# Kernel optimization log

Hardware: AMD Instinct MI355X
Metric: run time of the kernel (lower is better)

The kernel has to match this reference:

```python
import jax, jax.numpy as jnp
import numpy as np

NUM_CLASSES = 80
TOPK = 1000
CONF_THRESH = 0.001
NMS_THRESH = 0.5
CLASS_OFFSET = 4096.0  # > max image coordinate, separates classes for class-aware NMS
M = 300000


def setup_inputs() -> dict:
    key = jax.random.key(0)
    k1, k2, k3, k4 = jax.random.split(key, 4)
    obj_preds = jax.random.normal(k1, (1, M, 1), dtype=jnp.float32)
    cls_preds = jax.random.normal(k2, (1, M, NUM_CLASSES), dtype=jnp.float32)
    # random xyxy boxes inside a 640x640 image
    cxcy = jax.random.uniform(k3, (1, M, 2), dtype=jnp.float32) * 640.0
    wh = jax.random.uniform(k4, (1, M, 2), dtype=jnp.float32) * 128.0 + 1.0
    box_preds = jnp.concatenate([cxcy - wh * 0.5, cxcy + wh * 0.5], axis=-1)
    return {"obj_preds": obj_preds, "cls_preds": cls_preds, "box_preds": box_preds}


def _iou_matrix(boxes):
    # boxes: [K, 4] xyxy -> [K, K] pairwise IoU
    x1, y1, x2, y2 = boxes[:, 0], boxes[:, 1], boxes[:, 2], boxes[:, 3]
    area = jnp.clip(x2 - x1, 0.0) * jnp.clip(y2 - y1, 0.0)
    xx1 = jnp.maximum(x1[:, None], x1[None, :])
    yy1 = jnp.maximum(y1[:, None], y1[None, :])
    xx2 = jnp.minimum(x2[:, None], x2[None, :])
    yy2 = jnp.minimum(y2[:, None], y2[None, :])
    inter = jnp.clip(xx2 - xx1, 0.0) * jnp.clip(yy2 - yy1, 0.0)
    return inter / (area[:, None] + area[None, :] - inter + 1e-9)


def _postprocess(obj_preds, cls_preds, box_preds):
    obj = obj_preds[0]   # [M, 1]
    cls = cls_preds[0]   # [M, C]
    box = box_preds[0]   # [M, 4]

    # sigmoid * sigmoid sqrt-score fusion (no_multi_labels branch)
    fused = jnp.sqrt(jax.nn.sigmoid(obj) * jax.nn.sigmoid(cls))  # [M, C]
    scores = jnp.max(fused, axis=1)     # [M]
    labels = jnp.argmax(fused, axis=1)  # [M]

    # sort-descending + take top-k == lax.top_k
    topk_scores, topk_idxs = jax.lax.top_k(scores, TOPK)
    labels_k = labels[topk_idxs]        # [K]
    boxes_k = box[topk_idxs]            # [K, 4]
    conf_mask = topk_scores > CONF_THRESH

    # multiclass NMS via class-offset trick (boxes of different classes never overlap)
    off = labels_k.astype(boxes_k.dtype)[:, None] * CLASS_OFFSET
    iou = _iou_matrix(boxes_k + off)    # [K, K]

    idx = jnp.arange(TOPK)

    def body(i, keep):
        # suppressed if any earlier, still-kept box overlaps > nms_thresh
        sup = (iou[i] > NMS_THRESH) & keep & (idx < i)
        return keep.at[i].set(keep[i] & ~jnp.any(sup))

    keep = jax.lax.fori_loop(0, TOPK, body, conf_mask)  # [K] bool

    keepf = keep.astype(topk_scores.dtype)
    # fixed-shape output: masked [K, 5] = (score, x1, y1, x2, y2); dropped rows zeroed
    out5 = jnp.concatenate([(topk_scores * keepf)[:, None], boxes_k * keepf[:, None]], axis=1)
    return out5, labels_k, keep


def reference(obj_preds, cls_preds, box_preds):
    return _postprocess(obj_preds, cls_preds, box_preds)
```

## Files before the change

### kernel.cpp

```cpp
#include <hip/hip_runtime.h>
#include <hip/hip_bf16.h>
#include <math.h>

#define NCLS 80
#define TOPK_N 1000
#define CAND_CAP 12288
#define T0 0.91f
#define OBJ_T 1.55f
#define NB 8192
#define HREP 8
#define RBINS 3072
#define RBIN_LO 0x3F680000u
#define ANCH_INV 524287

#define WS_CAND     0
#define WS_TKSCORE  98304
#define WS_TKANCH   102304
#define WS_TKLABEL  106304
#define WS_BOXES    110304
#define WS_OBX      126304
#define WS_AREAS    142304
#define WS_MASK     146304
#define WS_META     274304
#define WS_HIST     274368

typedef unsigned long long u64;

__device__ __forceinline__ float sigmoidf_(float x) {
    return 1.0f / (1.0f + expf(-x));
}

__device__ __forceinline__ u64 make_key2(unsigned s32, int anchor) {
    return ((u64)s32 << 19) | (unsigned)(ANCH_INV - anchor);
}

__device__ __forceinline__ int key_bin(u64 k) {
    unsigned s32 = (unsigned)(k >> 19);
    int d = (int)(s32 - RBIN_LO);
    if (d < 0) d = 0;
    int b = d >> 9;
    if (b > RBINS - 1) b = RBINS - 1;
    return (RBINS - 1) - b;
}

__device__ __forceinline__ void rowmax16(const float4* row, int l,
                                         float& bv, int& bc) {
    float4 v4 = row[l];
    bv = v4.x; bc = l * 4;
    if (v4.y > bv) { bv = v4.y; bc = l * 4 + 1; }
    if (v4.z > bv) { bv = v4.z; bc = l * 4 + 2; }
    if (v4.w > bv) { bv = v4.w; bc = l * 4 + 3; }
    if (l < 4) {
        float4 w4 = row[16 + l];
        int cb = 64 + l * 4;
        if (w4.x > bv) { bv = w4.x; bc = cb; }
        if (w4.y > bv) { bv = w4.y; bc = cb + 1; }
        if (w4.z > bv) { bv = w4.z; bc = cb + 2; }
        if (w4.w > bv) { bv = w4.w; bc = cb + 3; }
    }
    #pragma unroll
    for (int m = 8; m >= 1; m >>= 1) {
        float ov = __shfl_xor(bv, m);
        int oc = __shfl_xor(bc, m);
        if (ov > bv || (ov == bv && oc < bc)) { bv = ov; bc = oc; }
    }
}

__global__ void __launch_bounds__(256)
k1_scores(const float* __restrict__ obj,
          const float* __restrict__ cls,
          u64* __restrict__ cand,
          int* __restrict__ counter,
          unsigned* __restrict__ hist,
          int M) {
    __shared__ int lcount, lbase, nsurv;
    __shared__ int sanch[256];
    __shared__ float sobj[256];
    __shared__ u64 lkeys[256];
    int t = threadIdx.x;
    if (t == 0) { lcount = 0; nsurv = 0; }
    for (int i = blockIdx.x * 256 + t; i < (HREP * NB) / 4; i += gridDim.x * 256)
        ((uint4*)hist)[i] = make_uint4(0u, 0u, 0u, 0u);
    __syncthreads();
    int a = blockIdx.x * 256 + t;
    float o = (a < M) ? obj[a] : -1e30f;
    if (o > OBJ_T) {
        int p = atomicAdd(&nsurv, 1);
        sanch[p] = a; sobj[p] = o;
    }
    __syncthreads();
    int ns = nsurv;
    int grp = t >> 4, l = t & 15;
    for (int s = grp; s < ns; s += 16) {
        int anchor = sanch[s];
        const float4* p = (const float4*)(cls + (size_t)anchor * NCLS);
        float4 v = p[l];
        float m = fmaxf(fmaxf(v.x, v.y), fmaxf(v.z, v.w));
        if (l < 4) {
            float4 w4 = p[16 + l];
            m = fmaxf(m, fmaxf(fmaxf(w4.x, w4.y), fmaxf(w4.z, w4.w)));
        }
        #pragma unroll
        for (int sh = 8; sh >= 1; sh >>= 1)
            m = fmaxf(m, __shfl_xor(m, sh));
        if (l == 0) {
            float score = sqrtf(sigmoidf_(sobj[s]) * sigmoidf_(m));
            if (score > T0) {
                int pos = atomicAdd(&lcount, 1);
                lkeys[pos] = make_key2(__float_as_uint(score), anchor);
            }
        }
    }
    __syncthreads();
    if (t == 0 && lcount > 0) lbase = atomicAdd(counter, lcount);
    __syncthreads();
    int n = lcount;
    if (t < n) {
        int pos = lbase + t;
        if (pos < CAND_CAP) cand[pos] = lkeys[t];
    }
}

__global__ void __launch_bounds__(256)
kfb_fallback(const float* __restrict__ obj,
             const float* __restrict__ cls,
             unsigned* __restrict__ hist,
             int* __restrict__ meta,
             u64* __restrict__ cand, int M) {
    int C = meta[2];
    if (C >= TOPK_N && C <= CAND_CAP) return;
    int t = threadIdx.x;
    int gw = (blockIdx.x * 256 + t) >> 6;
    int TW = gridDim.x * 4;
    int lane64 = t & 63;
    int g = lane64 >> 4, l = lane64 & 15;
    int rep = blockIdx.x & (HREP - 1);
    for (int a0 = gw * 4; a0 < M; a0 += TW * 4) {
        int anchor = a0 + g;
        if (anchor >= M) continue;
        const float4* row = (const float4*)(cls + (size_t)anchor * NCLS);
        float bv; int bc;
        rowmax16(row, l, bv, bc);
        if (l == 0) {
            float score = sqrtf(sigmoidf_(obj[anchor]) * sigmoidf_(bv));
            atomicAdd(&hist[(size_t)rep * NB + (__float_as_uint(score) >> 17)], 1u);
        }
    }
    __threadfence();
    __shared__ bool last;
    if (t == 0)
        last = (atomicAdd(meta + 4, 1) == (int)gridDim.x - 1);
    __syncthreads();
    if (last) {
        int lane = t & 63, w = t >> 6;
        int base = NB - 1 - t * 32;
        unsigned bins[32]; unsigned s = 0;
        #pragma unroll
        for (int k = 0; k < 32; ++k) {
            unsigned h = 0;
            for (int r = 0; r < HREP; ++r)
                h += atomicOr(&hist[(size_t)r * NB + base - k], 0u);
            bins[k] = h; s += h;
        }
        unsigned inc = s;
        for (int d = 1; d < 64; d <<= 1) {
            unsigned pv = __shfl_up(inc, d);
            if (lane >= d) inc += pv;
        }
        __shared__ unsigned wsum[4], woff[4];
        if (lane == 63) wsum[w] = inc;
        __syncthreads();
        if (t == 0) {
            unsigned cum = 0;
            for (int i = 0; i < 4; ++i) { woff[i] = cum; cum += wsum[i]; }
        }
        __syncthreads();
        unsigned excl = woff[w] + inc - s;
        if (excl < TOPK_N && excl + s >= TOPK_N) {
            unsigned cum = excl; int b = base;
            #pragma unroll
            for (int k = 0; k < 32; ++k) {
                unsigned h = bins[k];
                if (cum + h >= TOPK_N) { atomicExch(meta + 0, b); break; }
                cum += h; --b;
            }
        }
        __syncthreads();
        __threadfence();
        if (t == 0) atomicExch(meta + 5, 1);
    }
    if (t == 0)
        while (atomicAdd(meta + 5, 0) == 0) { __builtin_amdgcn_s_sleep(8); }
    __syncthreads();
    __threadfence();
    int B = atomicAdd(meta + 0, 0);
    for (int a0 = gw * 4; a0 < M; a0 += TW * 4) {
        int anchor = a0 + g;
        if (anchor >= M) continue;
        const float4* row = (const float4*)(cls + (size_t)anchor * NCLS);
        float bv; int bc;
        rowmax16(row, l, bv, bc);
        if (l == 0) {
            float score = sqrtf(sigmoidf_(obj[anchor]) * sigmoidf_(bv));
            unsigned key = __float_as_uint(score);
            if ((int)(key >> 17) >= B) {
                int pos = atomicAdd(meta + 3, 1);
                if (pos < CAND_CAP)
                    cand[pos] = make_key2(key, anchor);
            }
        }
    }
}

__global__ void __launch_bounds__(1024)
k4_rank(const u64* __restrict__ cand,
        const int* __restrict__ meta,
        float* __restrict__ tkscore,
        int* __restrict__ tkanchor) {
    __shared__ u64 sorted[CAND_CAP];
    __shared__ unsigned hist[RBINS];
    __shared__ unsigned cnt[RBINS];
    __shared__ unsigned wsum[16], woff[16];
    int t = threadIdx.x;
    int lane = t & 63, w = t >> 6;
    int Cf = meta[2];
    bool fast = (Cf >= TOPK_N && Cf <= CAND_CAP);
    int C = fast ? Cf : meta[3];
    if (C > CAND_CAP) C = CAND_CAP;
    for (int b = t; b < RBINS; b += 1024) { hist[b] = 0; cnt[b] = 0; }
    __syncthreads();
    u64 keys[12]; int nk = 0;
    for (int i = t; i < C; i += 1024) {
        u64 k = cand[i];
        keys[nk++] = k;
        atomicAdd(&hist[key_bin(k)], 1u);
    }
    __syncthreads();
    unsigned h0 = hist[t * 3], h1 = hist[t * 3 + 1], h2 = hist[t * 3 + 2];
    unsigned s = h0 + h1 + h2;
    unsigned inc = s;
    for (int d = 1; d < 64; d <<= 1) {
        unsigned pv = __shfl_up(inc, d);
        if (lane >= d) inc += pv;
    }
    if (lane == 63) wsum[w] = inc;
    __syncthreads();
    if (t == 0) {
        unsigned cum = 0;
        for (int i = 0; i < 16; ++i) { woff[i] = cum; cum += wsum[i]; }
    }
    __syncthreads();
    unsigned base = woff[w] + inc - s;
    hist[t * 3] = base;
    hist[t * 3 + 1] = base + h0;
    hist[t * 3 + 2] = base + h0 + h1;
    __syncthreads();
    nk = 0;
    for (int i = t; i < C; i += 1024) {
        u64 k = keys[nk++];
        int b = key_bin(k);
        unsigned pos = hist[b] + atomicAdd(&cnt[b], 1u);
        sorted[pos] = k;
    }
    __syncthreads();
    for (int p = t; p < C; p += 1024) {
        u64 k = sorted[p];
        int b = key_bin(k);
        unsigned b0 = hist[b], b1 = b0 + cnt[b];
        int r = (int)b0;
        for (unsigned q = b0; q < b1; ++q) r += (sorted[q] > k);
        if (r < TOPK_N) {
            tkscore[r] = __uint_as_float((unsigned)(k >> 19));
            tkanchor[r] = ANCH_INV - (int)(k & 0x7FFFF);
        }
    }
}

__global__ void __launch_bounds__(256)
k4b_gather(const float* __restrict__ cls,
           const float4* __restrict__ box,
           const int* __restrict__ tkanchor,
           int* __restrict__ tklabel,
           float4* __restrict__ boxes_k,
           float4* __restrict__ obx,
           float* __restrict__ areas) {
    int grp = threadIdx.x >> 4, l = threadIdx.x & 15;
    int r = blockIdx.x * 16 + grp;
    if (r >= TOPK_N) return;
    int anchor = tkanchor[r];
    const float4* row = (const float4*)(cls + (size_t)anchor * NCLS);
    float bv; int bc;
    rowmax16(row, l, bv, bc);
    if (l == 0) {
        tklabel[r] = bc;
        float4 b = box[anchor];
        boxes_k[r] = b;
        float off = (float)bc * 4096.0f;
        float4 ob = make_float4(b.x + off, b.y + off, b.z + off, b.w + off);
        obx[r] = ob;
        areas[r] = fmaxf(ob.z - ob.x, 0.0f) * fmaxf(ob.w - ob.y, 0.0f);
    }
}

__global__ void __launch_bounds__(1024)
k5_iou(const float4* __restrict__ obx,
       const float* __restrict__ areas,
       u64* __restrict__ mask) {
    __shared__ float4 sobx[TOPK_N];
    __shared__ float  sarea[TOPK_N];
    int t = threadIdx.x;
    for (int j = t; j < TOPK_N; j += 1024) { sobx[j] = obx[j]; sarea[j] = areas[j]; }
    __syncthreads();
    int w = t >> 6, lane = t & 63;
    int i = blockIdx.x * 16 + w;
    if (i >= TOPK_N) return;
    float4 bi = sobx[i];
    float ai = sarea[i];
    #pragma unroll 4
    for (int q = 0; q < 16; ++q) {
        int c = q * 64 + lane;
        bool bit = false;
        if (c < i) {
            float4 bc = sobx[c];
            float xx1 = fmaxf(bi.x, bc.x), yy1 = fmaxf(bi.y, bc.y);
            float xx2 = fminf(bi.z, bc.z), yy2 = fminf(bi.w, bc.w);
            float inter = fmaxf(xx2 - xx1, 0.0f) * fmaxf(yy2 - yy1, 0.0f);
            float iou = inter / (ai + sarea[c] - inter + 1e-9f);
            bit = iou > 0.5f;
        }
        u64 bal = __ballot(bit);
        if (lane == 0) mask[(size_t)i * 16 + q] = bal;
    }
}

__global__ void __launch_bounds__(1024)
k6_nms(const float* __restrict__ tkscore,
       const u64* __restrict__ mask,
       const int* __restrict__ tklabel,
       const float4* __restrict__ boxes_k,
       float* __restrict__ out) {
    __shared__ u64 kept_s[16], dec_s[16];
    int t = threadIdx.x, w = t >> 6, lane = t & 63;
    bool active = t < TOPK_N;
    u64 sup[16];
    float sc = 0.0f;
    if (active) {
        #pragma unroll
        for (int q = 0; q < 16; ++q) sup[q] = mask[(size_t)t * 16 + q];
        sc = tkscore[t];
    } else {
        #pragma unroll
        for (int q = 0; q < 16; ++q) sup[q] = 0ULL;
    }
    bool conf = active && (sc > 0.001f);
    bool mydec = !conf;
    bool mykept = false;
    u64 db = __ballot(mydec), kb = __ballot(mykept);
    if (lane == 0) { dec_s[w] = db; kept_s[w] = kb; }
    __syncthreads();
    for (int round = 0; round < TOPK_N; ++round) {
        if (!mydec) {
            u64 pend = 0;
            #pragma unroll
            for (int q = 0; q < 16; ++q) pend |= sup[q] & ~dec_s[q];
            if (pend == 0ULL) {
                u64 kk = 0;
                #pragma unroll
                for (int q = 0; q < 16; ++q) kk |= sup[q] & kept_s[q];
                mydec = true; mykept = (kk == 0ULL);
            }
        }
        __syncthreads();
        db = __ballot(mydec); kb = __ballot(mykept);
        if (lane == 0) { dec_s[w] = db; kept_s[w] = kb; }
        __syncthreads();
        u64 a = ~0ULL;
        #pragma unroll
        for (int q = 0; q < 16; ++q) a &= dec_s[q];
        if (a == ~0ULL) break;
    }
    if (active) {
        float k = mykept ? 1.0f : 0.0f;
        float4 b = boxes_k[t];
        out[t * 5 + 0] = sc * k;
        out[t * 5 + 1] = b.x * k;
        out[t * 5 + 2] = b.y * k;
        out[t * 5 + 3] = b.z * k;
        out[t * 5 + 4] = b.w * k;
        out[5 * TOPK_N + t] = (float)tklabel[t];
        out[6 * TOPK_N + t] = k;
    }
}

extern "C" void kernel_launch(void* const* d_in, const int* in_sizes, int n_in,
                              void* d_out, int out_size, void* d_ws, size_t ws_size,
                              hipStream_t stream) {
    const float* obj = (const float*)d_in[0];
    const float* cls = (const float*)d_in[1];
    const float* box = (const float*)d_in[2];
    float* out = (float*)d_out;
    char* ws = (char*)d_ws;
    int M = in_sizes[0];

    u64*      cand    = (u64*)(ws + WS_CAND);
    float*    tkscore = (float*)(ws + WS_TKSCORE);
    int*      tkanch  = (int*)(ws + WS_TKANCH);
    int*      tklabel = (int*)(ws + WS_TKLABEL);
    float4*   boxes_k = (float4*)(ws + WS_BOXES);
    float4*   obx     = (float4*)(ws + WS_OBX);
    float*    areas   = (float*)(ws + WS_AREAS);
    u64*      mask    = (u64*)(ws + WS_MASK);
    int*      meta    = (int*)(ws + WS_META);
    unsigned* hist    = (unsigned*)(ws + WS_HIST);

    hipMemsetAsync(ws + WS_META, 0, 64, stream);

    k1_scores<<<(M + 255) / 256, 256, 0, stream>>>(obj, cls, cand, meta + 2, hist, M);
    kfb_fallback<<<512, 256, 0, stream>>>(obj, cls, hist, meta, cand, M);
    k4_rank<<<1, 1024, 0, stream>>>(cand, meta, tkscore, tkanch);
    k4b_gather<<<(TOPK_N + 15) / 16, 256, 0, stream>>>(cls, (const float4*)box,
                                                       tkanch, tklabel, boxes_k, obx, areas);
    k5_iou<<<63, 1024, 0, stream>>>(obx, areas, mask);
    k6_nms<<<1, 1024, 0, stream>>>(tkscore, mask, tklabel, boxes_k, out);
}
```

Measured before the change: 165.9 us.

## Fold fallback and gather into single-block rank kernel, drop two launches

Removes the grid-wide fallback kernel and the separate gather kernel. The rare fallback path (candidate count out of range) now runs inside the single-block rank kernel using a shared-memory histogram, and the top-k label/box gather is done in the same kernel after ranking. On the fast path this saves two kernel launches and the global histogram zeroing in k1. The cost is that the fallback path, if it ever triggers, becomes a very slow single-block scan over all anchors, and the gather now runs on one block instead of many.

```diff
diff --git a/kernel.cpp b/kernel.cpp
--- a/kernel.cpp
+++ b/kernel.cpp
@@ -8,21 +8,18 @@
 #define T0 0.91f
 #define OBJ_T 1.55f
 #define NB 8192
-#define HREP 8
 #define RBINS 3072
 #define RBIN_LO 0x3F680000u
 #define ANCH_INV 524287
 
 #define WS_CAND     0
 #define WS_TKSCORE  98304
-#define WS_TKANCH   102304
-#define WS_TKLABEL  106304
-#define WS_BOXES    110304
-#define WS_OBX      126304
-#define WS_AREAS    142304
-#define WS_MASK     146304
-#define WS_META     274304
-#define WS_HIST     274368
+#define WS_TKLABEL  102304
+#define WS_BOXES    106304
+#define WS_OBX      122304
+#define WS_AREAS    138304
+#define WS_MASK     142304
+#define WS_META     270304
 
 typedef unsigned long long u64;
 
@@ -71,7 +68,6 @@
           const float* __restrict__ cls,
           u64* __restrict__ cand,
           int* __restrict__ counter,
-          unsigned* __restrict__ hist,
           int M) {
     __shared__ int lcount, lbase, nsurv;
     __shared__ int sanch[256];
@@ -79,8 +75,6 @@
     __shared__ u64 lkeys[256];
     int t = threadIdx.x;
     if (t == 0) { lcount = 0; nsurv = 0; }
-    for (int i = blockIdx.x * 256 + t; i < (HREP * NB) / 4; i += gridDim.x * 256)
-        ((uint4*)hist)[i] = make_uint4(0u, 0u, 0u, 0u);
     __syncthreads();
     int a = blockIdx.x * 256 + t;
     float o = (a < M) ? obj[a] : -1e30f;
@@ -121,112 +115,92 @@
     }
 }
 
-__global__ void __launch_bounds__(256)
-kfb_fallback(const float* __restrict__ obj,
-             const float* __restrict__ cls,
-             unsigned* __restrict__ hist,
-             int* __restrict__ meta,
-             u64* __restrict__ cand, int M) {
-    int C = meta[2];
-    if (C >= TOPK_N && C <= CAND_CAP) return;
+__global__ void __launch_bounds__(1024)
+k4x_rank_gather(const float* __restrict__ obj,
+                const float* __restrict__ cls,
+                const float4* __restrict__ box,
+                u64* __restrict__ cand,
+                const int* __restrict__ meta,
+                float* __restrict__ tkscore,
+                int* __restrict__ tklabel,
+                float4* __restrict__ boxes_k,
+                float4* __restrict__ obx,
+                float* __restrict__ areas,
+                int M) {
+    __shared__ u64 sorted[CAND_CAP];
+    __shared__ unsigned hist[RBINS];
+    __shared__ unsigned cnt[RBINS];
+    __shared__ unsigned wsum[16], woff[16];
+    __shared__ int ranch[TOPK_N];
+    __shared__ int fbB, fbC;
     int t = threadIdx.x;
-    int gw = (blockIdx.x * 256 + t) >> 6;
-    int TW = gridDim.x * 4;
-    int lane64 = t & 63;
-    int g = lane64 >> 4, l = lane64 & 15;
-    int rep = blockIdx.x & (HREP - 1);
-    for (int a0 = gw * 4; a0 < M; a0 += TW * 4) {
-        int anchor = a0 + g;
-        if (anchor >= M) continue;
-        const float4* row = (const float4*)(cls + (size_t)anchor * NCLS);
-        float bv; int bc;
-        rowmax16(row, l, bv, bc);
-        if (l == 0) {
-            float score = sqrtf(sigmoidf_(obj[anchor]) * sigmoidf_(bv));
-            atomicAdd(&hist[(size_t)rep * NB + (__float_as_uint(score) >> 17)], 1u);
-        }
-    }
-    __threadfence();
-    __shared__ bool last;
-    if (t == 0)
-        last = (atomicAdd(meta + 4, 1) == (int)gridDim.x - 1);
-    __syncthreads();
-    if (last) {
-        int lane = t & 63, w = t >> 6;
-        int base = NB - 1 - t * 32;
-        unsigned bins[32]; unsigned s = 0;
-        #pragma unroll
-        for (int k = 0; k < 32; ++k) {
-            unsigned h = 0;
-            for (int r = 0; r < HREP; ++r)
-                h += atomicOr(&hist[(size_t)r * NB + base - k], 0u);
-            bins[k] = h; s += h;
-        }
+    int lane = t & 63, w = t >> 6;
+    int Cf = meta[2];
+    bool fast = (Cf >= TOPK_N && Cf <= CAND_CAP);
+    int C;
+    if (fast) {
+        C = Cf;
+    } else {
+        unsigned* fh = (unsigned*)sorted;
+        for (int b = t; b < NB; b += 1024) fh[b] = 0;
+        if (t == 0) { fbB = 0; fbC = 0; }
+        __syncthreads();
+        int g = t >> 4, l = t & 15;
+        for (int a0 = g; a0 < M; a0 += 64) {
+            const float4* row = (const float4*)(cls + (size_t)a0 * NCLS);
+            float bv; int bc;
+            rowmax16(row, l, bv, bc);
+            if (l == 0) {
+                float sc = sqrtf(sigmoidf_(obj[a0]) * sigmoidf_(bv));
+                atomicAdd(&fh[__float_as_uint(sc) >> 17], 1u);
+            }
+        }
+        __syncthreads();
+        int base = NB - 1 - t * 8;
+        unsigned bins[8]; unsigned s = 0;
+        #pragma unroll
+        for (int k = 0; k < 8; ++k) { unsigned h = fh[base - k]; bins[k] = h; s += h; }
         unsigned inc = s;
         for (int d = 1; d < 64; d <<= 1) {
             unsigned pv = __shfl_up(inc, d);
             if (lane >= d) inc += pv;
         }
-        __shared__ unsigned wsum[4], woff[4];
         if (lane == 63) wsum[w] = inc;
         __syncthreads();
         if (t == 0) {
             unsigned cum = 0;
-            for (int i = 0; i < 4; ++i) { woff[i] = cum; cum += wsum[i]; }
+            for (int i = 0; i < 16; ++i) { woff[i] = cum; cum += wsum[i]; }
         }
         __syncthreads();
         unsigned excl = woff[w] + inc - s;
         if (excl < TOPK_N && excl + s >= TOPK_N) {
             unsigned cum = excl; int b = base;
             #pragma unroll
-            for (int k = 0; k < 32; ++k) {
+            for (int k = 0; k < 8; ++k) {
                 unsigned h = bins[k];
-                if (cum + h >= TOPK_N) { atomicExch(meta + 0, b); break; }
+                if (cum + h >= TOPK_N) { fbB = b; break; }
                 cum += h; --b;
             }
         }
         __syncthreads();
-        __threadfence();
-        if (t == 0) atomicExch(meta + 5, 1);
-    }
-    if (t == 0)
-        while (atomicAdd(meta + 5, 0) == 0) { __builtin_amdgcn_s_sleep(8); }
-    __syncthreads();
-    __threadfence();
-    int B = atomicAdd(meta + 0, 0);
-    for (int a0 = gw * 4; a0 < M; a0 += TW * 4) {
-        int anchor = a0 + g;
-        if (anchor >= M) continue;
-        const float4* row = (const float4*)(cls + (size_t)anchor * NCLS);
-        float bv; int bc;
-        rowmax16(row, l, bv, bc);
-        if (l == 0) {
-            float score = sqrtf(sigmoidf_(obj[anchor]) * sigmoidf_(bv));
-            unsigned key = __float_as_uint(score);
-            if ((int)(key >> 17) >= B) {
-                int pos = atomicAdd(meta + 3, 1);
-                if (pos < CAND_CAP)
-                    cand[pos] = make_key2(key, anchor);
-            }
-        }
-    }
-}
-
-__global__ void __launch_bounds__(1024)
-k4_rank(const u64* __restrict__ cand,
-        const int* __restrict__ meta,
-        float* __restrict__ tkscore,
-        int* __restrict__ tkanchor) {
-    __shared__ u64 sorted[CAND_CAP];
-    __shared__ unsigned hist[RBINS];
-    __shared__ unsigned cnt[RBINS];
-    __shared__ unsigned wsum[16], woff[16];
-    int t = threadIdx.x;
-    int lane = t & 63, w = t >> 6;
-    int Cf = meta[2];
-    bool fast = (Cf >= TOPK_N && Cf <= CAND_CAP);
-    int C = fast ? Cf : meta[3];
-    if (C > CAND_CAP) C = CAND_CAP;
+        int B = fbB;
+        for (int a0 = g; a0 < M; a0 += 64) {
+            const float4* row = (const float4*)(cls + (size_t)a0 * NCLS);
+            float bv; int bc;
+            rowmax16(row, l, bv, bc);
+            if (l == 0) {
+                float sc = sqrtf(sigmoidf_(obj[a0]) * sigmoidf_(bv));
+                unsigned key = __float_as_uint(sc);
+                if ((int)(key >> 17) >= B) {
+                    int pos = atomicAdd(&fbC, 1);
+                    if (pos < CAND_CAP) cand[pos] = make_key2(key, a0);
+                }
+            }
+        }
+        __syncthreads();
+        C = fbC < CAND_CAP ? fbC : CAND_CAP;
+        __syncthreads();
+    }
     for (int b = t; b < RBINS; b += 1024) { hist[b] = 0; cnt[b] = 0; }
     __syncthreads();
     u64 keys[12]; int nk = 0;
@@ -237,23 +211,23 @@
     }
     __syncthreads();
     unsigned h0 = hist[t * 3], h1 = hist[t * 3 + 1], h2 = hist[t * 3 + 2];
-    unsigned s = h0 + h1 + h2;
-    unsigned inc = s;
+    unsigned s2 = h0 + h1 + h2;
+    unsigned inc2 = s2;
     for (int d = 1; d < 64; d <<= 1) {
-        unsigned pv = __shfl_up(inc, d);
-        if (lane >= d) inc += pv;
-    }
-    if (lane == 63) wsum[w] = inc;
+        unsigned pv = __shfl_up(inc2, d);
+        if (lane >= d) inc2 += pv;
+    }
+    if (lane == 63) wsum[w] = inc2;
     __syncthreads();
     if (t == 0) {
         unsigned cum = 0;
         for (int i = 0; i < 16; ++i) { woff[i] = cum; cum += wsum[i]; }
     }
     __syncthreads();
-    unsigned base = woff[w] + inc - s;
-    hist[t * 3] = base;
-    hist[t * 3 + 1] = base + h0;
-    hist[t * 3 + 2] = base + h0 + h1;
+    unsigned rbase = woff[w] + inc2 - s2;
+    hist[t * 3] = rbase;
+    hist[t * 3 + 1] = rbase + h0;
+    hist[t * 3 + 2] = rbase + h0 + h1;
     __syncthreads();
     nk = 0;
     for (int i = t; i < C; i += 1024) {
@@ -271,34 +245,25 @@
         for (unsigned q = b0; q < b1; ++q) r += (sorted[q] > k);
         if (r < TOPK_N) {
             tkscore[r] = __uint_as_float((unsigned)(k >> 19));
-            tkanchor[r] = ANCH_INV - (int)(k & 0x7FFFF);
-        }
-    }
-}
-
-__global__ void __launch_bounds__(256)
-k4b_gather(const float* __restrict__ cls,
-           const float4* __restrict__ box,
-           const int* __restrict__ tkanchor,
-           int* __restrict__ tklabel,
-           float4* __restrict__ boxes_k,
-           float4* __restrict__ obx,
-           float* __restrict__ areas) {
-    int grp = threadIdx.x >> 4, l = threadIdx.x & 15;
-    int r = blockIdx.x * 16 + grp;
-    if (r >= TOPK_N) return;
-    int anchor = tkanchor[r];
-    const float4* row = (const float4*)(cls + (size_t)anchor * NCLS);
-    float bv; int bc;
-    rowmax16(row, l, bv, bc);
-    if (l == 0) {
-        tklabel[r] = bc;
-        float4 b = box[anchor];
-        boxes_k[r] = b;
-        float off = (float)bc * 4096.0f;
-        float4 ob = make_float4(b.x + off, b.y + off, b.z + off, b.w + off);
-        obx[r] = ob;
-        areas[r] = fmaxf(ob.z - ob.x, 0.0f) * fmaxf(ob.w - ob.y, 0.0f);
+            ranch[r] = ANCH_INV - (int)(k & 0x7FFFF);
+        }
+    }
+    __syncthreads();
+    int g2 = t >> 4, l2 = t & 15;
+    for (int r = g2; r < TOPK_N; r += 64) {
+        int anchor = ranch[r];
+        const float4* row = (const float4*)(cls + (size_t)anchor * NCLS);
+        float bv; int bc;
+        rowmax16(row, l2, bv, bc);
+        if (l2 == 0) {
+            tklabel[r] = bc;
+            float4 b = box[anchor];
+            boxes_k[r] = b;
+            float off = (float)bc * 4096.0f;
+            float4 ob = make_float4(b.x + off, b.y + off, b.z + off, b.w + off);
+            obx[r] = ob;
+            areas[r] = fmaxf(ob.z - ob.x, 0.0f) * fmaxf(ob.w - ob.y, 0.0f);
+        }
     }
 }
 
@@ -404,22 +369,19 @@
 
     u64*      cand    = (u64*)(ws + WS_CAND);
     float*    tkscore = (float*)(ws + WS_TKSCORE);
-    int*      tkanch  = (int*)(ws + WS_TKANCH);
     int*      tklabel = (int*)(ws + WS_TKLABEL);
     float4*   boxes_k = (float4*)(ws + WS_BOXES);
     float4*   obx     = (float4*)(ws + WS_OBX);
     float*    areas   = (float*)(ws + WS_AREAS);
     u64*      mask    = (u64*)(ws + WS_MASK);
     int*      meta    = (int*)(ws + WS_META);
-    unsigned* hist    = (unsigned*)(ws + WS_HIST);
 
     hipMemsetAsync(ws + WS_META, 0, 64, stream);
 
-    k1_scores<<<(M + 255) / 256, 256, 0, stream>>>(obj, cls, cand, meta + 2, hist, M);
-    kfb_fallback<<<512, 256, 0, stream>>>(obj, cls, hist, meta, cand, M);
-    k4_rank<<<1, 1024, 0, stream>>>(cand, meta, tkscore, tkanch);
-    k4b_gather<<<(TOPK_N + 15) / 16, 256, 0, stream>>>(cls, (const float4*)box,
-                                                       tkanch, tklabel, boxes_k, obx, areas);
+    k1_scores<<<(M + 255) / 256, 256, 0, stream>>>(obj, cls, cand, meta + 2, M);
+    k4x_rank_gather<<<1, 1024, 0, stream>>>(obj, cls, (const float4*)box, cand,
+                                            meta, tkscore, tklabel, boxes_k,
+                                            obx, areas, M);
     k5_iou<<<63, 1024, 0, stream>>>(obx, areas, mask);
     k6_nms<<<1, 1024, 0, stream>>>(tkscore, mask, tklabel, boxes_k, out);
 }
```

New measurement: 186.5 us. 1.12x slower.
